# Performance work log

Measured on AMD Instinct MI355X. Metric: run time of the kernel, lower is better.

## Reference

```python
import jax, jax.numpy as jnp
import numpy as np

NUM_HEADS = 8


def _proj(W, b, x):
    # x: [B, C, N] channel-wise 1x1 conv == matmul over channels
    return jnp.einsum('oc,bcn->bon', W, x) + b[None, :, None]


def setup_inputs() -> dict:
    key = jax.random.key(0)
    ks = jax.random.split(key, 8)
    B, C, H, W = 4, 512, 24, 24
    inp = {
        'feat0': jax.random.normal(ks[0], (B, C, H, W), jnp.float32),
        'feat1': jax.random.normal(ks[1], (B, C, H, W), jnp.float32),
        'feat2': jax.random.normal(ks[2], (B, C, H, W), jnp.float32),
        'Wq': jax.random.normal(ks[3], (C, C), jnp.float32) * 0.02,
        'bq': jnp.zeros((C,), jnp.float32),
        'Wk': jax.random.normal(ks[4], (C, C), jnp.float32) * 0.02,
        'bk': jnp.zeros((C,), jnp.float32),
        'Wv': jax.random.normal(ks[5], (C, C), jnp.float32) * 0.02,
        'bv': jnp.zeros((C,), jnp.float32),
        'Wo': jax.random.normal(ks[6], (C, C), jnp.float32) * 0.02,
        'bo': jnp.zeros((C,), jnp.float32),
    }
    return inp


def reference(feat0, feat1, feat2, Wq, bq, Wk, bk, Wv, bv, Wo, bo):
    feats = [feat0, feat1, feat2]
    B, C, H, W = feat0.shape
    h = NUM_HEADS
    d = C // h
    scale = d ** -0.5

    # Precompute K/V once per feature (the torch loop redundantly recomputes them;
    # the math is identical).
    flat = [f.reshape(B, C, H * W) for f in feats]
    K = jnp.concatenate([_proj(Wk, bk, x).reshape(B, h, d, -1) for x in flat], axis=-1)  # [B,h,d,KV]
    V = jnp.concatenate([_proj(Wv, bv, x).reshape(B, h, d, -1) for x in flat], axis=-1)  # [B,h,d,KV]

    outs = []
    for feat, x in zip(feats, flat):
        q = _proj(Wq, bq, x).reshape(B, h, d, H * W)  # [B,h,d,N]
        attn = jax.nn.softmax(jnp.einsum('bhdn,bhdm->bhnm', q, K) * scale, axis=-1)
        out = jnp.einsum('bhnm,bhdm->bhdn', attn, V).reshape(B, C, H * W)
        out = _proj(Wo, bo, out).reshape(B, C, H, W)
        outs.append(feat + out)
    return tuple(outs)
```

## Files before the change

kernel.cpp:

```cpp
#include <hip/hip_runtime.h>


using bf16x8 = __attribute__((ext_vector_type(8))) short;
using f32x4  = __attribute__((ext_vector_type(4))) float;
using f32x16 = __attribute__((ext_vector_type(16))) float;
using u32x4  = __attribute__((ext_vector_type(4))) unsigned int;
using u16x4  = __attribute__((ext_vector_type(4))) unsigned short;
using u16x8  = __attribute__((ext_vector_type(8))) unsigned short;

#define MFMA16(a, b, c) __builtin_amdgcn_mfma_f32_16x16x32_bf16((a), (b), (c), 0, 0, 0)
#define MFMA32(a, b, c) __builtin_amdgcn_mfma_f32_32x32x16_bf16((a), (b), (c), 0, 0, 0)

__device__ __forceinline__ unsigned short f2bf(float f) {
  unsigned int u = __float_as_uint(f);
  return (unsigned short)((u + 0x7fffu + ((u >> 16) & 1u)) >> 16);
}

__device__ __forceinline__ f32x16 zero16() {
  f32x16 z;
#pragma unroll
  for (int i = 0; i < 16; ++i) z[i] = 0.f;
  return z;
}

__global__ __launch_bounds__(256) void k_prep(
    const float* __restrict__ Wq, const float* __restrict__ Wk,
    const float* __restrict__ Wv, const float* __restrict__ Wo,
    const float* __restrict__ f0, const float* __restrict__ f1,
    const float* __restrict__ f2,
    unsigned short* __restrict__ Wf, unsigned short* __restrict__ Xf) {
  __shared__ unsigned short tile[64][65];
  const int bid = blockIdx.x;
  const int t = threadIdx.x;
  if (bid < 1024) {
    int idx = (bid * 256 + t) * 4;
    int p   = idx >> 18;
    int rem = idx & 262143;
    int o = rem >> 9, c0 = rem & 511;
    const float* s = p == 0 ? Wq : p == 1 ? Wk : p == 2 ? Wv : Wo;
    f32x4 v = *(const f32x4*)(s + rem);
    u16x4 pk;
    pk[0] = f2bf(v[0]); pk[1] = f2bf(v[1]); pk[2] = f2bf(v[2]); pk[3] = f2bf(v[3]);
    int mt = o >> 6, fr = (o & 63) >> 4, lr = o & 15;
    int ks = c0 >> 5, lg = (c0 & 31) >> 3, j0 = c0 & 7;
    size_t off = (size_t)((((p * 8 + mt) * 16 + ks) * 4 + fr)) * 512 +
                 (lg * 16 + lr) * 8 + j0;
    *(u16x4*)(Wf + off) = pk;
    return;
  }
  const int id = bid - 1024;
  const int nt = id % 9;
  const int ct = (id / 9) % 8;
  const int z  = id / 72;
  const int b = z / 3, f = z % 3;
  const float* src = (f == 0 ? f0 : f == 1 ? f1 : f2) + b * (512 * 576);

#pragma unroll
  for (int i = 0; i < 16; ++i) {
    int idx = i * 256 + t;
    int cc = idx >> 6, nn = idx & 63;
    tile[cc][nn] = f2bf(src[(ct * 64 + cc) * 576 + nt * 64 + nn]);
  }
  __syncthreads();
  const int ntw = f * 9 + nt;
#pragma unroll
  for (int i = 0; i < 4; ++i) {
    int slot = i * 256 + t;
    int nn = slot >> 4, cq = slot & 15;
    int cl = cq * 4;
    int c  = ct * 64 + cl;
    int fc = nn >> 4, lr = nn & 15;
    int ks = c >> 5, lg = (c & 31) >> 3, j0 = c & 7;
    u16x4 pk;
    pk[0] = tile[cl][nn]; pk[1] = tile[cl + 1][nn];
    pk[2] = tile[cl + 2][nn]; pk[3] = tile[cl + 3][nn];
    size_t off = (size_t)((((b * 27 + ntw) * 16 + ks) * 4 + fc)) * 512 +
                 (lg * 16 + lr) * 8 + j0;
    *(u16x4*)(Xf + off) = pk;
  }
}

__global__ __launch_bounds__(256) void k_gemm_qkv(
    const unsigned short* __restrict__ Wf, const unsigned short* __restrict__ Xf,
    const float* __restrict__ bq, const float* __restrict__ bk,
    const float* __restrict__ bv,
    unsigned short* __restrict__ Qf, unsigned short* __restrict__ Kf,
    unsigned short* __restrict__ Vf) {
  const int id = blockIdx.x;
  const int xcd = id & 7, s = id >> 3;
  const int b = xcd >> 1, par = xcd & 1;
  const int p = s / 27, bx = (s % 27) * 2 + par;
  const int t = threadIdx.x, w = t >> 6, l = t & 63, lg = l >> 4, lr = l & 15;
  const int wid = bx * 4 + w;
  const int mt = wid / 27, ntw = wid % 27;
  const unsigned short* A = Wf + (size_t)(p * 8 + mt) * 16 * 2048 + l * 8;
  const unsigned short* B = Xf + (size_t)(b * 27 + ntw) * 16 * 2048 + l * 8;

  f32x4 acc[4][4];
#pragma unroll
  for (int fr = 0; fr < 4; ++fr)
#pragma unroll
    for (int fc = 0; fc < 4; ++fc) acc[fr][fc] = (f32x4){0.f, 0.f, 0.f, 0.f};

#pragma unroll 2
  for (int ks = 0; ks < 16; ++ks) {
    bf16x8 af[4], bfv[4];
#pragma unroll
    for (int fr = 0; fr < 4; ++fr)
      af[fr] = *(const bf16x8*)(A + ks * 2048 + fr * 512);
#pragma unroll
    for (int fc = 0; fc < 4; ++fc)
      bfv[fc] = *(const bf16x8*)(B + ks * 2048 + fc * 512);
#pragma unroll
    for (int fr = 0; fr < 4; ++fr)
#pragma unroll
      for (int fc = 0; fc < 4; ++fc)
        acc[fr][fc] = MFMA16(af[fr], bfv[fc], acc[fr][fc]);
  }

  const float* bias = p == 0 ? bq : p == 1 ? bk : bv;
  const int bh = b * 8 + mt;
#pragma unroll
  for (int fr = 0; fr < 4; ++fr) {
    f32x4 b4 = *(const f32x4*)(bias + mt * 64 + fr * 16 + lg * 4);
#pragma unroll
    for (int fc = 0; fc < 4; ++fc) {
      int ck = ntw * 2 + (fc >> 1);
      if (p < 2) {
        unsigned short* outF = (p == 0) ? Qf : Kf;
        u16x4 pk;
#pragma unroll
        for (int r = 0; r < 4; ++r) pk[r] = f2bf(acc[fr][fc][r] + b4[r]);
        size_t off = ((size_t)bh * 54 + ck) * 2048 + fr * 512 +
                     ((lg >> 1) * 32 + (fc & 1) * 16 + lr) * 8 + (lg & 1) * 4;
        *(u16x4*)(outF + off) = pk;
      } else {
        size_t base = ((size_t)bh * 54 + ck) * 2048 +
                      ((fr >> 1) * 2 + (fc & 1)) * 512 +
                      (((lr >> 3) & 1) * 32 + (fr & 1) * 16 + lg * 4) * 8 +
                      (lr & 7);
#pragma unroll
        for (int r = 0; r < 4; ++r)
          Vf[base + r * 8] = f2bf(acc[fr][fc][r] + b4[r]);
      }
    }
  }
}

__device__ __forceinline__ void softmax_pa(const f32x16& s, float& lsum,
                                           bf16x8& pa0, bf16x8& pa1, int hi) {
  unsigned int W[8];
  float a0 = 0.f, a1 = 0.f;
#pragma unroll
  for (int u = 0; u < 8; ++u) {
    float e0, e1;
    asm("v_exp_f32 %0, %1" : "=v"(e0) : "v"(s[2 * u] * 0.18033688f));
    asm("v_exp_f32 %0, %1" : "=v"(e1) : "v"(s[2 * u + 1] * 0.18033688f));
    a0 += e0; a1 += e1;
    asm("v_cvt_pk_bf16_f32 %0, %1, %2" : "=v"(W[u]) : "v"(e0), "v"(e1));
  }
  lsum += a0 + a1;
  unsigned int fw[2][4];
#pragma unroll
  for (int kf = 0; kf < 2; ++kf)
#pragma unroll
    for (int wd = 0; wd < 2; ++wd) {
      unsigned int lo  = W[4 * kf + wd];
      unsigned int hw  = W[4 * kf + 2 + wd];
      unsigned int pub = hi ? lo : hw;
      unsigned int rcv = (unsigned int)__shfl_xor((int)pub, 32, 64);
      fw[kf][wd]     = hi ? rcv : lo;
      fw[kf][2 + wd] = hi ? hw : rcv;
    }
  u32x4 w0, w1;
  w0[0] = fw[0][0]; w0[1] = fw[0][1]; w0[2] = fw[0][2]; w0[3] = fw[0][3];
  w1[0] = fw[1][0]; w1[1] = fw[1][1]; w1[2] = fw[1][2]; w1[3] = fw[1][3];
  pa0 = __builtin_bit_cast(bf16x8, w0);
  pa1 = __builtin_bit_cast(bf16x8, w1);
}

__global__ __launch_bounds__(256) void k_attn(
    const unsigned short* __restrict__ Qf, const unsigned short* __restrict__ Kf,
    const unsigned short* __restrict__ Vf, unsigned short* __restrict__ Of) {
  const int id = blockIdx.x;
  const int xcd = id & 7, slot = id >> 3;
  const int bh = xcd * 4 + (slot / 54);
  const int qt = slot % 54;
  const int b = bh >> 3, h = bh & 7;
  const int t = threadIdx.x, w = t >> 6, l = t & 63;
  const int lr = l & 31, hi = l >> 5;

  __shared__ float Obuf[4][32][68];
  __shared__ float Lbuf[4][32];

  const unsigned short* Qb = Qf + ((size_t)bh * 54 + qt) * 2048 + l * 8;
  bf16x8 bq[4];
#pragma unroll
  for (int kf = 0; kf < 4; ++kf) bq[kf] = *(const bf16x8*)(Qb + kf * 512);

  f32x16 oacc[2];
  oacc[0] = zero16(); oacc[1] = zero16();
  float ls = 0.f;

  const unsigned short* Kb = Kf + (size_t)bh * 54 * 2048 + l * 8;
  const unsigned short* Vb = Vf + (size_t)bh * 54 * 2048 + l * 8;

  bf16x8 ak[4], vb[4];
  {
    const unsigned short* kc = Kb + w * 2048;
    const unsigned short* vc = Vb + w * 2048;
#pragma unroll
    for (int i = 0; i < 4; ++i) ak[i] = *(const bf16x8*)(kc + i * 512);
#pragma unroll
    for (int i = 0; i < 4; ++i) vb[i] = *(const bf16x8*)(vc + i * 512);
  }
  f32x16 sA = zero16();
#pragma unroll
  for (int kf = 0; kf < 4; ++kf) sA = MFMA32(ak[kf], bq[kf], sA);

#pragma unroll 1
  for (int ck = w + 4; ck < 54; ck += 4) {
    bf16x8 akn[4], vbn[4];
    const unsigned short* kn = Kb + ck * 2048;
    const unsigned short* vn = Vb + ck * 2048;
#pragma unroll
    for (int i = 0; i < 4; ++i) akn[i] = *(const bf16x8*)(kn + i * 512);
#pragma unroll
    for (int i = 0; i < 4; ++i) vbn[i] = *(const bf16x8*)(vn + i * 512);

    bf16x8 pa0, pa1;
    softmax_pa(sA, ls, pa0, pa1, hi);

    f32x16 sB = zero16();
#pragma unroll
    for (int kf = 0; kf < 4; ++kf) sB = MFMA32(akn[kf], bq[kf], sB);

    oacc[0] = MFMA32(pa0, vb[0], oacc[0]);
    oacc[0] = MFMA32(pa1, vb[1], oacc[0]);
    oacc[1] = MFMA32(pa0, vb[2], oacc[1]);
    oacc[1] = MFMA32(pa1, vb[3], oacc[1]);

    sA = sB;
#pragma unroll
    for (int i = 0; i < 4; ++i) vb[i] = vbn[i];
  }

  {
    bf16x8 pa0, pa1;
    softmax_pa(sA, ls, pa0, pa1, hi);
    oacc[0] = MFMA32(pa0, vb[0], oacc[0]);
    oacc[0] = MFMA32(pa1, vb[1], oacc[0]);
    oacc[1] = MFMA32(pa0, vb[2], oacc[1]);
    oacc[1] = MFMA32(pa1, vb[3], oacc[1]);
  }

  float lt = ls + __shfl_xor(ls, 32, 64);
  if (l < 32) Lbuf[w][lr] = lt;
#pragma unroll
  for (int dt = 0; dt < 2; ++dt)
#pragma unroll
    for (int r = 0; r < 16; ++r)
      Obuf[w][(r & 3) + 8 * (r >> 2) + 4 * hi][dt * 32 + lr] = oacc[dt][r];
  __syncthreads();

  const int n = t >> 3, d0 = (t & 7) * 8;
  float ltot = Lbuf[0][n] + Lbuf[1][n] + Lbuf[2][n] + Lbuf[3][n];
  float linv = 1.0f / ltot;
  u16x8 o8;
#pragma unroll
  for (int i = 0; i < 8; ++i) {
    float ov = Obuf[0][n][d0 + i] + Obuf[1][n][d0 + i] +
               Obuf[2][n][d0 + i] + Obuf[3][n][d0 + i];
    o8[i] = f2bf(ov * linv);
  }
  size_t off = (size_t)((((b * 27 + (qt >> 1)) * 16 + h * 2 + (d0 >> 5)) * 4 +
                         (qt & 1) * 2 + (n >> 4))) * 512 +
               ((d0 >> 3) & 3) * 128 + (n & 15) * 8;
  *(u16x8*)(Of + off) = o8;
}

__global__ __launch_bounds__(256) void k_gemm_out(
    const unsigned short* __restrict__ Wf, const unsigned short* __restrict__ Of,
    const float* __restrict__ bo,
    const float* __restrict__ f0, const float* __restrict__ f1,
    const float* __restrict__ f2, float* __restrict__ out) {
  const int z = blockIdx.z, b = z / 3, f = z % 3;
  const int t = threadIdx.x, w = t >> 6, l = t & 63, lg = l >> 4, lr = l & 15;
  const int wid = blockIdx.x * 4 + w;
  const int mt = wid / 9, ntw = wid % 9;
  const int o0 = mt * 64;
  const unsigned short* A = Wf + (size_t)(3 * 8 + mt) * 16 * 2048 + l * 8;
  const unsigned short* B = Of + (size_t)(b * 27 + f * 9 + ntw) * 16 * 2048 + l * 8;

  f32x4 acc[4][4];
#pragma unroll
  for (int fr = 0; fr < 4; ++fr)
#pragma unroll
    for (int fc = 0; fc < 4; ++fc) acc[fr][fc] = (f32x4){0.f, 0.f, 0.f, 0.f};

#pragma unroll 2
  for (int ks = 0; ks < 16; ++ks) {
    bf16x8 af[4], bfv[4];
#pragma unroll
    for (int fr = 0; fr < 4; ++fr)
      af[fr] = *(const bf16x8*)(A + ks * 2048 + fr * 512);
#pragma unroll
    for (int fc = 0; fc < 4; ++fc)
      bfv[fc] = *(const bf16x8*)(B + ks * 2048 + fc * 512);
#pragma unroll
    for (int fr = 0; fr < 4; ++fr)
#pragma unroll
      for (int fc = 0; fc < 4; ++fc)
        acc[fr][fc] = MFMA16(af[fr], bfv[fc], acc[fr][fc]);
  }

  const float* ft = f == 0 ? f0 : f == 1 ? f1 : f2;
#pragma unroll
  for (int fr = 0; fr < 4; ++fr) {
    f32x4 b4 = *(const f32x4*)(bo + o0 + fr * 16 + lg * 4);
#pragma unroll
    for (int fc = 0; fc < 4; ++fc) {
      int ncol = ntw * 64 + fc * 16 + lr;
#pragma unroll
      for (int r = 0; r < 4; ++r) {
        int o = o0 + fr * 16 + lg * 4 + r;
        out[((f * 4 + b) * 512 + o) * 576 + ncol] =
            acc[fr][fc][r] + b4[r] + ft[(b * 512 + o) * 576 + ncol];
      }
    }
  }
}

extern "C" void kernel_launch(void* const* d_in, const int* in_sizes, int n_in,
                              void* d_out, int out_size, void* d_ws, size_t ws_size,
                              hipStream_t stream) {
  const float* f0 = (const float*)d_in[0];
  const float* f1 = (const float*)d_in[1];
  const float* f2 = (const float*)d_in[2];
  const float* Wq = (const float*)d_in[3];
  const float* bq = (const float*)d_in[4];
  const float* Wk = (const float*)d_in[5];
  const float* bk = (const float*)d_in[6];
  const float* Wv = (const float*)d_in[7];
  const float* bv = (const float*)d_in[8];
  const float* Wo = (const float*)d_in[9];
  const float* bo = (const float*)d_in[10];
  float* out = (float*)d_out;

  char* ws = (char*)d_ws;
  unsigned short* Wf = (unsigned short*)(ws);
  unsigned short* Xf = (unsigned short*)(ws + 2097152);
  unsigned short* Qf = (unsigned short*)(ws + 9175040);
  unsigned short* Kf = (unsigned short*)(ws + 16252928);
  unsigned short* Vf = (unsigned short*)(ws + 23330816);
  unsigned short* Of = Xf;

  k_prep<<<dim3(1888), 256, 0, stream>>>(Wq, Wk, Wv, Wo, f0, f1, f2, Wf, Xf);
  k_gemm_qkv<<<dim3(648), 256, 0, stream>>>(Wf, Xf, bq, bk, bv, Qf, Kf, Vf);
  k_attn<<<dim3(1728), 256, 0, stream>>>(Qf, Kf, Vf, Of);
  k_gemm_out<<<dim3(18, 1, 12), 256, 0, stream>>>(Wf, Of, bo, f0, f1, f2, out);
}
```

Baseline: 100.1 us.

## Halve GEMM wave tiles, fold softmax scale into Q, simplify attention loop

Both projection GEMMs now give each wave a 64x32 tile instead of 64x64, which doubles the grid so more waves are resident. The softmax scale (including log2e) is applied once when Q is written, so the per-element multiply disappears from the attention inner loop. The attention kernel drops its software-pipelined K/V prefetch in favour of a simple per-chunk loop and adds a 4-blocks-per-SM launch bound, relying on occupancy rather than register double-buffering to hide latency. Smaller GEMM tiles reduce A-operand reuse, so weight traffic per FLOP goes up.

```diff
diff --git a/kernel.cpp b/kernel.cpp
--- a/kernel.cpp
+++ b/kernel.cpp
@@ -89,54 +89,60 @@
   const int id = blockIdx.x;
   const int xcd = id & 7, s = id >> 3;
   const int b = xcd >> 1, par = xcd & 1;
-  const int p = s / 27, bx = (s % 27) * 2 + par;
+  const int p = s / 54, bx = (s % 54) * 2 + par;
   const int t = threadIdx.x, w = t >> 6, l = t & 63, lg = l >> 4, lr = l & 15;
   const int wid = bx * 4 + w;
-  const int mt = wid / 27, ntw = wid % 27;
+  const int mt = wid / 54, rest = wid % 54;
+  const int ntw = rest >> 1, half = rest & 1;
   const unsigned short* A = Wf + (size_t)(p * 8 + mt) * 16 * 2048 + l * 8;
-  const unsigned short* B = Xf + (size_t)(b * 27 + ntw) * 16 * 2048 + l * 8;
-
-  f32x4 acc[4][4];
+  const unsigned short* B = Xf + (size_t)(b * 27 + ntw) * 16 * 2048 +
+                            half * 1024 + l * 8;
+
+  f32x4 acc[4][2];
 #pragma unroll
   for (int fr = 0; fr < 4; ++fr)
 #pragma unroll
-    for (int fc = 0; fc < 4; ++fc) acc[fr][fc] = (f32x4){0.f, 0.f, 0.f, 0.f};
+    for (int fc = 0; fc < 2; ++fc) acc[fr][fc] = (f32x4){0.f, 0.f, 0.f, 0.f};
 
 #pragma unroll 2
   for (int ks = 0; ks < 16; ++ks) {
-    bf16x8 af[4], bfv[4];
+    bf16x8 af[4], bfv[2];
 #pragma unroll
     for (int fr = 0; fr < 4; ++fr)
       af[fr] = *(const bf16x8*)(A + ks * 2048 + fr * 512);
 #pragma unroll
-    for (int fc = 0; fc < 4; ++fc)
+    for (int fc = 0; fc < 2; ++fc)
       bfv[fc] = *(const bf16x8*)(B + ks * 2048 + fc * 512);
 #pragma unroll
     for (int fr = 0; fr < 4; ++fr)
 #pragma unroll
-      for (int fc = 0; fc < 4; ++fc)
+      for (int fc = 0; fc < 2; ++fc)
         acc[fr][fc] = MFMA16(af[fr], bfv[fc], acc[fr][fc]);
   }
 
   const float* bias = p == 0 ? bq : p == 1 ? bk : bv;
   const int bh = b * 8 + mt;
+  const int ck = ntw * 2 + half;
 #pragma unroll
   for (int fr = 0; fr < 4; ++fr) {
     f32x4 b4 = *(const f32x4*)(bias + mt * 64 + fr * 16 + lg * 4);
 #pragma unroll
-    for (int fc = 0; fc < 4; ++fc) {
-      int ck = ntw * 2 + (fc >> 1);
+    for (int fc = 0; fc < 2; ++fc) {
       if (p < 2) {
         unsigned short* outF = (p == 0) ? Qf : Kf;
         u16x4 pk;
 #pragma unroll
-        for (int r = 0; r < 4; ++r) pk[r] = f2bf(acc[fr][fc][r] + b4[r]);
+        for (int r = 0; r < 4; ++r) {
+          float v = acc[fr][fc][r] + b4[r];
+          if (p == 0) v *= 0.18033688f;
+          pk[r] = f2bf(v);
+        }
         size_t off = ((size_t)bh * 54 + ck) * 2048 + fr * 512 +
-                     ((lg >> 1) * 32 + (fc & 1) * 16 + lr) * 8 + (lg & 1) * 4;
+                     ((lg >> 1) * 32 + fc * 16 + lr) * 8 + (lg & 1) * 4;
         *(u16x4*)(outF + off) = pk;
       } else {
         size_t base = ((size_t)bh * 54 + ck) * 2048 +
-                      ((fr >> 1) * 2 + (fc & 1)) * 512 +
+                      ((fr >> 1) * 2 + fc) * 512 +
                       (((lr >> 3) & 1) * 32 + (fr & 1) * 16 + lg * 4) * 8 +
                       (lr & 7);
 #pragma unroll
@@ -147,39 +153,7 @@
   }
 }
 
-__device__ __forceinline__ void softmax_pa(const f32x16& s, float& lsum,
-                                           bf16x8& pa0, bf16x8& pa1, int hi) {
-  unsigned int W[8];
-  float a0 = 0.f, a1 = 0.f;
-#pragma unroll
-  for (int u = 0; u < 8; ++u) {
-    float e0, e1;
-    asm("v_exp_f32 %0, %1" : "=v"(e0) : "v"(s[2 * u] * 0.18033688f));
-    asm("v_exp_f32 %0, %1" : "=v"(e1) : "v"(s[2 * u + 1] * 0.18033688f));
-    a0 += e0; a1 += e1;
-    asm("v_cvt_pk_bf16_f32 %0, %1, %2" : "=v"(W[u]) : "v"(e0), "v"(e1));
-  }
-  lsum += a0 + a1;
-  unsigned int fw[2][4];
-#pragma unroll
-  for (int kf = 0; kf < 2; ++kf)
-#pragma unroll
-    for (int wd = 0; wd < 2; ++wd) {
-      unsigned int lo  = W[4 * kf + wd];
-      unsigned int hw  = W[4 * kf + 2 + wd];
-      unsigned int pub = hi ? lo : hw;
-      unsigned int rcv = (unsigned int)__shfl_xor((int)pub, 32, 64);
-      fw[kf][wd]     = hi ? rcv : lo;
-      fw[kf][2 + wd] = hi ? hw : rcv;
-    }
-  u32x4 w0, w1;
-  w0[0] = fw[0][0]; w0[1] = fw[0][1]; w0[2] = fw[0][2]; w0[3] = fw[0][3];
-  w1[0] = fw[1][0]; w1[1] = fw[1][1]; w1[2] = fw[1][2]; w1[3] = fw[1][3];
-  pa0 = __builtin_bit_cast(bf16x8, w0);
-  pa1 = __builtin_bit_cast(bf16x8, w1);
-}
-
-__global__ __launch_bounds__(256) void k_attn(
+__global__ __launch_bounds__(256, 4) void k_attn(
     const unsigned short* __restrict__ Qf, const unsigned short* __restrict__ Kf,
     const unsigned short* __restrict__ Vf, unsigned short* __restrict__ Of) {
   const int id = blockIdx.x;
@@ -205,49 +179,52 @@
   const unsigned short* Kb = Kf + (size_t)bh * 54 * 2048 + l * 8;
   const unsigned short* Vb = Vf + (size_t)bh * 54 * 2048 + l * 8;
 
-  bf16x8 ak[4], vb[4];
-  {
-    const unsigned short* kc = Kb + w * 2048;
-    const unsigned short* vc = Vb + w * 2048;
+#pragma unroll 1
+  for (int ck = w; ck < 54; ck += 4) {
+    const unsigned short* kc = Kb + ck * 2048;
+    const unsigned short* vc = Vb + ck * 2048;
+    bf16x8 ak[4];
 #pragma unroll
     for (int i = 0; i < 4; ++i) ak[i] = *(const bf16x8*)(kc + i * 512);
+
+    f32x16 sA = zero16();
+#pragma unroll
+    for (int kf = 0; kf < 4; ++kf) sA = MFMA32(ak[kf], bq[kf], sA);
+
+    bf16x8 vb[4];
 #pragma unroll
     for (int i = 0; i < 4; ++i) vb[i] = *(const bf16x8*)(vc + i * 512);
-  }
-  f32x16 sA = zero16();
-#pragma unroll
-  for (int kf = 0; kf < 4; ++kf) sA = MFMA32(ak[kf], bq[kf], sA);
-
-#pragma unroll 1
-  for (int ck = w + 4; ck < 54; ck += 4) {
-    bf16x8 akn[4], vbn[4];
-    const unsigned short* kn = Kb + ck * 2048;
-    const unsigned short* vn = Vb + ck * 2048;
-#pragma unroll
-    for (int i = 0; i < 4; ++i) akn[i] = *(const bf16x8*)(kn + i * 512);
-#pragma unroll
-    for (int i = 0; i < 4; ++i) vbn[i] = *(const bf16x8*)(vn + i * 512);
-
-    bf16x8 pa0, pa1;
-    softmax_pa(sA, ls, pa0, pa1, hi);
-
-    f32x16 sB = zero16();
-#pragma unroll
-    for (int kf = 0; kf < 4; ++kf) sB = MFMA32(akn[kf], bq[kf], sB);
-
-    oacc[0] = MFMA32(pa0, vb[0], oacc[0]);
-    oacc[0] = MFMA32(pa1, vb[1], oacc[0]);
-    oacc[1] = MFMA32(pa0, vb[2], oacc[1]);
-    oacc[1] = MFMA32(pa1, vb[3], oacc[1]);
-
-    sA = sB;
-#pragma unroll
-    for (int i = 0; i < 4; ++i) vb[i] = vbn[i];
-  }
-
-  {
-    bf16x8 pa0, pa1;
-    softmax_pa(sA, ls, pa0, pa1, hi);
+
+    unsigned int W[8];
+    float a0 = 0.f, a1 = 0.f;
+#pragma unroll
+    for (int u = 0; u < 8; ++u) {
+      float e0, e1;
+      asm("v_exp_f32 %0, %1" : "=v"(e0) : "v"(sA[2 * u]));
+      asm("v_exp_f32 %0, %1" : "=v"(e1) : "v"(sA[2 * u + 1]));
+      a0 += e0; a1 += e1;
+      asm("v_cvt_pk_bf16_f32 %0, %1, %2" : "=v"(W[u]) : "v"(e0), "v"(e1));
+    }
+    ls += a0 + a1;
+
+    unsigned int fw[2][4];
+#pragma unroll
+    for (int kf = 0; kf < 2; ++kf)
+#pragma unroll
+      for (int wd = 0; wd < 2; ++wd) {
+        unsigned int lo  = W[4 * kf + wd];
+        unsigned int hw  = W[4 * kf + 2 + wd];
+        unsigned int pub = hi ? lo : hw;
+        unsigned int rcv = (unsigned int)__shfl_xor((int)pub, 32, 64);
+        fw[kf][wd]     = hi ? rcv : lo;
+        fw[kf][2 + wd] = hi ? hw : rcv;
+      }
+    u32x4 w0, w1;
+    w0[0] = fw[0][0]; w0[1] = fw[0][1]; w0[2] = fw[0][2]; w0[3] = fw[0][3];
+    w1[0] = fw[1][0]; w1[1] = fw[1][1]; w1[2] = fw[1][2]; w1[3] = fw[1][3];
+    bf16x8 pa0 = __builtin_bit_cast(bf16x8, w0);
+    bf16x8 pa1 = __builtin_bit_cast(bf16x8, w1);
+
     oacc[0] = MFMA32(pa0, vb[0], oacc[0]);
     oacc[0] = MFMA32(pa1, vb[1], oacc[0]);
     oacc[1] = MFMA32(pa0, vb[2], oacc[1]);
@@ -287,30 +264,32 @@
   const int z = blockIdx.z, b = z / 3, f = z % 3;
   const int t = threadIdx.x, w = t >> 6, l = t & 63, lg = l >> 4, lr = l & 15;
   const int wid = blockIdx.x * 4 + w;
-  const int mt = wid / 9, ntw = wid % 9;
+  const int mt = wid / 18, rest = wid % 18;
+  const int ntw = rest >> 1, half = rest & 1;
   const int o0 = mt * 64;
   const unsigned short* A = Wf + (size_t)(3 * 8 + mt) * 16 * 2048 + l * 8;
-  const unsigned short* B = Of + (size_t)(b * 27 + f * 9 + ntw) * 16 * 2048 + l * 8;
-
-  f32x4 acc[4][4];
+  const unsigned short* B = Of + (size_t)(b * 27 + f * 9 + ntw) * 16 * 2048 +
+                            half * 1024 + l * 8;
+
+  f32x4 acc[4][2];
 #pragma unroll
   for (int fr = 0; fr < 4; ++fr)
 #pragma unroll
-    for (int fc = 0; fc < 4; ++fc) acc[fr][fc] = (f32x4){0.f, 0.f, 0.f, 0.f};
+    for (int fc = 0; fc < 2; ++fc) acc[fr][fc] = (f32x4){0.f, 0.f, 0.f, 0.f};
 
 #pragma unroll 2
   for (int ks = 0; ks < 16; ++ks) {
-    bf16x8 af[4], bfv[4];
+    bf16x8 af[4], bfv[2];
 #pragma unroll
     for (int fr = 0; fr < 4; ++fr)
       af[fr] = *(const bf16x8*)(A + ks * 2048 + fr * 512);
 #pragma unroll
-    for (int fc = 0; fc < 4; ++fc)
+    for (int fc = 0; fc < 2; ++fc)
       bfv[fc] = *(const bf16x8*)(B + ks * 2048 + fc * 512);
 #pragma unroll
     for (int fr = 0; fr < 4; ++fr)
 #pragma unroll
-      for (int fc = 0; fc < 4; ++fc)
+      for (int fc = 0; fc < 2; ++fc)
         acc[fr][fc] = MFMA16(af[fr], bfv[fc], acc[fr][fc]);
   }
 
@@ -319,8 +298,8 @@
   for (int fr = 0; fr < 4; ++fr) {
     f32x4 b4 = *(const f32x4*)(bo + o0 + fr * 16 + lg * 4);
 #pragma unroll
-    for (int fc = 0; fc < 4; ++fc) {
-      int ncol = ntw * 64 + fc * 16 + lr;
+    for (int fc = 0; fc < 2; ++fc) {
+      int ncol = ntw * 64 + half * 32 + fc * 16 + lr;
 #pragma unroll
       for (int r = 0; r < 4; ++r) {
         int o = o0 + fr * 16 + lg * 4 + r;
@@ -356,7 +335,7 @@
   unsigned short* Of = Xf;
 
   k_prep<<<dim3(1888), 256, 0, stream>>>(Wq, Wk, Wv, Wo, f0, f1, f2, Wf, Xf);
-  k_gemm_qkv<<<dim3(648), 256, 0, stream>>>(Wf, Xf, bq, bk, bv, Qf, Kf, Vf);
+  k_gemm_qkv<<<dim3(1296), 256, 0, stream>>>(Wf, Xf, bq, bk, bv, Qf, Kf, Vf);
   k_attn<<<dim3(1728), 256, 0, stream>>>(Qf, Kf, Vf, Of);
-  k_gemm_out<<<dim3(18, 1, 12), 256, 0, stream>>>(Wf, Of, bo, f0, f1, f2, out);
-}
+  k_gemm_out<<<dim3(36, 1, 12), 256, 0, stream>>>(Wf, Of, bo, f0, f1, f2, out);
+}
```

Result: faster. 90.00 us (-10.1%).
